# Kernel optimization log

Measured on AMD Instinct MI355X. Metric: run time of the kernel, lower is better.

Reference implementation:

```python
import jax, jax.numpy as jnp
import numpy as np

B, S, D, H, E = 8, 196, 768, 12, 8
HD = D // H  # 64
FF = 4 * D   # 3072
EPS = 1e-5


def setup_inputs() -> dict:
    key = jax.random.key(0)
    ks = jax.random.split(key, 12)
    s = 0.02
    inp = {
        'x': jax.random.normal(ks[0], (B, S, D), jnp.float32),
        'ln1_g': jnp.ones((D,), jnp.float32),
        'ln1_b': jnp.zeros((D,), jnp.float32),
        'Wq': jax.random.normal(ks[1], (D, D), jnp.float32) * s,
        'bq': jnp.zeros((D,), jnp.float32),
        'Wk': jax.random.normal(ks[2], (D, HD), jnp.float32) * s,
        'bk': jnp.zeros((HD,), jnp.float32),
        'Wv': jax.random.normal(ks[3], (D, HD), jnp.float32) * s,
        'bv': jnp.zeros((HD,), jnp.float32),
        'ln2_g': jnp.ones((D,), jnp.float32),
        'ln2_b': jnp.zeros((D,), jnp.float32),
        'Wg': jax.random.normal(ks[4], (D, E), jnp.float32) * s,
        'bg': jnp.zeros((E,), jnp.float32),
        'W1': jax.random.normal(ks[5], (E, D, FF), jnp.float32) * s,
        'b1': jnp.zeros((E, FF), jnp.float32),
        'W2': jax.random.normal(ks[6], (E, FF, D), jnp.float32) * s,
        'b2': jnp.zeros((E, D), jnp.float32),
    }
    return inp


def _layernorm(x, g, b):
    mu = jnp.mean(x, axis=-1, keepdims=True)
    var = jnp.var(x, axis=-1, keepdims=True)
    return (x - mu) * jax.lax.rsqrt(var + EPS) * g + b


def _rotate_half(x):
    x1, x2 = jnp.split(x, 2, axis=-1)
    return jnp.concatenate((-x2, x1), axis=-1)


def _rope(seq_len):
    inv_freq = 1.0 / (10000.0 ** (jnp.arange(0, HD, 2, dtype=jnp.float32) / HD))
    freqs = jnp.arange(seq_len, dtype=jnp.float32)[:, None] * inv_freq[None, :]
    emb = jnp.concatenate((freqs, freqs), axis=-1)  # [S, HD]
    return emb[None, :, None, :]  # [1, S, 1, HD]


def _attention(x, Wq, bq, Wk, bk, Wv, bv):
    b, s, _ = x.shape
    q = (x @ Wq + bq).reshape(b, s, H, HD)
    k = (x @ Wk + bk).reshape(b, s, 1, HD)
    v = (x @ Wv + bv).reshape(b, s, 1, HD)
    k = jnp.broadcast_to(k, (b, s, H, HD))
    v = jnp.broadcast_to(v, (b, s, H, HD))
    pe = _rope(s)
    cos, sin = jnp.cos(pe), jnp.sin(pe)
    q = q * cos + _rotate_half(q) * sin
    k = k * cos + _rotate_half(k) * sin
    scale = HD ** -0.5
    # NOTE: faithful to source -- matmul over the last two dims of [b,s,h,d],
    # i.e. attention across HEADS, not sequence positions.
    attn = jnp.einsum('bshd,bsgd->bshg', q, k) * scale
    attn = jax.nn.softmax(attn, axis=-1)
    out = jnp.einsum('bshg,bsgd->bshd', attn, v)
    return out.reshape(b, s, H * HD)


def _moe(x, Wg, bg, W1, b1, W2, b2):
    b, s, d = x.shape
    xt = x.reshape(-1, d)  # [T, D]
    gates = jax.nn.softmax(xt @ Wg + bg, axis=-1)
    top1 = jnp.argmax(gates, axis=-1)  # topk(k=2)[:,0] == argmax
    out = jnp.zeros_like(xt)
    for e in range(E):  # small fixed expert count
        h = jax.nn.gelu(xt @ W1[e] + b1[e], approximate=False)
        y = h @ W2[e] + b2[e]
        out = jnp.where((top1 == e)[:, None], y, out)
    return out.reshape(b, s, d)


def reference(x, ln1_g, ln1_b, Wq, bq, Wk, bk, Wv, bv, ln2_g, ln2_b, Wg, bg, W1, b1, W2, b2):
    res = x
    h = _layernorm(x, ln1_g, ln1_b)
    h = _attention(h, Wq, bq, Wk, bk, Wv, bv)
    x = res + h
    res = x
    h = _layernorm(x, ln2_g, ln2_b)
    h = _moe(h, Wg, bg, W1, b1, W2, b2)
    return res + h
```

## Files before the change

kernel.cpp:

```cpp
#include <hip/hip_runtime.h>
#include <hip/hip_bf16.h>


typedef unsigned short u16;
typedef short bf16x8_t __attribute__((ext_vector_type(8)));
typedef unsigned short u16x4_t __attribute__((ext_vector_type(4)));
typedef float f32x4_t  __attribute__((ext_vector_type(4)));

#define T_TOK 1568
#define DM 768
#define HD 64
#define FF 3072
#define NE 8

#define OFF_CNT   0
#define OFF_BUCK  256
#define OFF_V     (OFF_BUCK + NE*T_TOK*4)
#define OFF_H1    (OFF_V + T_TOK*HD*4)
#define OFF_H2    (OFF_H1 + T_TOK*DM*2)
#define OFF_HMID  (OFF_H2 + T_TOK*DM*2)

__device__ __forceinline__ u16 f2bf(float f) {
    return __builtin_bit_cast(u16, __float2bfloat16(f));
}
__device__ __forceinline__ float bf2f(u16 h) {
    unsigned u = ((unsigned)h) << 16;
    return __builtin_bit_cast(float, u);
}
__device__ __forceinline__ float gelu_f(float x) {
    return 0.5f * x * (1.0f + erff(x * 0.70710678118654752440f));
}

#define SFENCE() __builtin_amdgcn_sched_barrier(0)
#define RAW_BAR() __builtin_amdgcn_s_barrier()

__global__ __launch_bounds__(64) void k_ln1(const float* __restrict__ x,
                                            const float* __restrict__ g1,
                                            const float* __restrict__ b1,
                                            u16* __restrict__ h1) {
    int t = blockIdx.x, lane = threadIdx.x;
    const float* xp = x + (size_t)t * DM;
    f32x4_t xv[3];
    float s = 0.0f;
#pragma unroll
    for (int i = 0; i < 3; i++) {
        xv[i] = *(const f32x4_t*)&xp[4 * lane + 256 * i];
        s += xv[i][0] + xv[i][1] + xv[i][2] + xv[i][3];
    }
#pragma unroll
    for (int m = 1; m < 64; m <<= 1) s += __shfl_xor(s, m);
    float mu = s * (1.0f / DM);
    float vs = 0.0f;
#pragma unroll
    for (int i = 0; i < 3; i++)
#pragma unroll
        for (int m = 0; m < 4; m++) { float d = xv[i][m] - mu; vs += d * d; }
#pragma unroll
    for (int m = 1; m < 64; m <<= 1) vs += __shfl_xor(vs, m);
    float rs = rsqrtf(vs * (1.0f / DM) + 1e-5f);
    u16* hp = h1 + (size_t)t * DM;
#pragma unroll
    for (int i = 0; i < 3; i++) {
        int c = 4 * lane + 256 * i;
        f32x4_t gg = *(const f32x4_t*)&g1[c];
        f32x4_t bb = *(const f32x4_t*)&b1[c];
        u16x4_t hb;
#pragma unroll
        for (int m = 0; m < 4; m++) hb[m] = f2bf((xv[i][m] - mu) * rs * gg[m] + bb[m]);
        *(u16x4_t*)&hp[c] = hb;
    }
}

__global__ __launch_bounds__(256) void k_vproj(
        const u16* __restrict__ h1, const float* __restrict__ Wv,
        const float* __restrict__ bv, float* __restrict__ vws) {
    __shared__ __align__(16) u16 Bh[64 * 72];
    __shared__ __align__(16) u16 Bl[64 * 72];
    int m0 = blockIdx.x * 64;
    int tid = threadIdx.x, lane = tid & 63, wid = tid >> 6;
    int bn = tid & 63, bkg = tid >> 6;
    int lr = lane & 15, q = lane >> 4;
    int row = m0 + wid * 16 + lr;
    if (row >= T_TOK) row = T_TOK - 1;
    const u16* ap = h1 + (size_t)row * DM;

    f32x4_t acc[4];
#pragma unroll
    for (int ni = 0; ni < 4; ni++) acc[ni] = (f32x4_t){0.f, 0.f, 0.f, 0.f};

    bf16x8_t aP[2], aQ[2];
    float bP[16], bQ[16];

#define G_LOAD_A(SA, KT) { \
    int k0_ = (KT) * 64; \
    SA[0] = *(const bf16x8_t*)&ap[k0_ + q * 8]; \
    SA[1] = *(const bf16x8_t*)&ap[k0_ + 32 + q * 8]; \
}
#define G_LOAD_B(SB, KT) { \
    const float* bp_ = Wv + (size_t)((KT) * 64 + bkg * 16) * HD + bn; \
    _Pragma("unroll") \
    for (int kk = 0; kk < 16; kk++) SB[kk] = bp_[(size_t)kk * HD]; \
}
#define STORE_B(SB) { \
    bf16x8_t h0_, h1_, l0_, l1_; \
    _Pragma("unroll") \
    for (int kk = 0; kk < 8; kk++) { \
        float w0 = SB[kk], w1 = SB[kk + 8]; \
        u16 hh0 = f2bf(w0), hh1 = f2bf(w1); \
        h0_[kk] = (short)hh0; h1_[kk] = (short)hh1; \
        l0_[kk] = (short)f2bf(w0 - bf2f(hh0)); \
        l1_[kk] = (short)f2bf(w1 - bf2f(hh1)); \
    } \
    *(bf16x8_t*)&Bh[bn * 72 + bkg * 16] = h0_; \
    *(bf16x8_t*)&Bh[bn * 72 + bkg * 16 + 8] = h1_; \
    *(bf16x8_t*)&Bl[bn * 72 + bkg * 16] = l0_; \
    *(bf16x8_t*)&Bl[bn * 72 + bkg * 16 + 8] = l1_; \
}
#define MFMA_TILE(SA) { \
    _Pragma("unroll") \
    for (int s = 0; s < 2; s++) { \
        bf16x8_t bh_[4], bl_[4]; \
        _Pragma("unroll") \
        for (int ni = 0; ni < 4; ni++) { \
            bh_[ni] = *(const bf16x8_t*)&Bh[(ni * 16 + lr) * 72 + s * 32 + q * 8]; \
            bl_[ni] = *(const bf16x8_t*)&Bl[(ni * 16 + lr) * 72 + s * 32 + q * 8]; \
        } \
        _Pragma("unroll") \
        for (int ni = 0; ni < 4; ni++) { \
            acc[ni] = __builtin_amdgcn_mfma_f32_16x16x32_bf16( \
                SA[s], bh_[ni], acc[ni], 0, 0, 0); \
            acc[ni] = __builtin_amdgcn_mfma_f32_16x16x32_bf16( \
                SA[s], bl_[ni], acc[ni], 0, 0, 0); \
        } \
    } \
}
#define PHASE(SA, SB, PKT) { \
    SFENCE(); RAW_BAR(); SFENCE(); \
    STORE_B(SB) \
    asm volatile("s_waitcnt lgkmcnt(0)" ::: "memory"); \
    SFENCE(); RAW_BAR(); SFENCE(); \
    if ((PKT) < 12) G_LOAD_B(SB, PKT) \
    MFMA_TILE(SA) \
    if ((PKT) < 12) G_LOAD_A(SA, PKT) \
}

    G_LOAD_A(aP, 0) G_LOAD_B(bP, 0)
    G_LOAD_A(aQ, 1) G_LOAD_B(bQ, 1)
    for (int kt = 0; kt < 12; kt += 2) {
        PHASE(aP, bP, kt + 2)
        PHASE(aQ, bQ, kt + 3)
    }
#undef G_LOAD_A
#undef G_LOAD_B
#undef STORE_B
#undef MFMA_TILE
#undef PHASE

#pragma unroll
    for (int ni = 0; ni < 4; ni++) {
        float bb = bv[ni * 16 + lr];
#pragma unroll
        for (int r = 0; r < 4; r++) {
            int i = m0 + wid * 16 + q * 4 + r;
            if (i < T_TOK) vws[(size_t)i * HD + ni * 16 + lr] = acc[ni][r] + bb;
        }
    }
}

__global__ __launch_bounds__(64) void k_gate(
        const float* __restrict__ x, const float* __restrict__ vws,
        const float* __restrict__ g2, const float* __restrict__ b2g,
        const float* __restrict__ Wg, const float* __restrict__ bg,
        const float* __restrict__ b2moe,
        u16* __restrict__ h2, float* __restrict__ out,
        int* __restrict__ cnt, int* __restrict__ buck) {
    int t = blockIdx.x, lane = threadIdx.x;
    int sl = lane & 15;
    const float* xp = x + (size_t)t * DM;
    f32x4_t xv[3];
    f32x4_t vv = *(const f32x4_t*)&vws[(size_t)t * HD + 4 * sl];
    float s2 = 0.0f;
#pragma unroll
    for (int i = 0; i < 3; i++) {
        xv[i] = *(const f32x4_t*)&xp[4 * lane + 256 * i];
#pragma unroll
        for (int m = 0; m < 4; m++) { xv[i][m] += vv[m]; s2 += xv[i][m]; }
    }
#pragma unroll
    for (int m = 1; m < 64; m <<= 1) s2 += __shfl_xor(s2, m);
    float mu2 = s2 * (1.0f / DM);
    float vs2 = 0.0f;
#pragma unroll
    for (int i = 0; i < 3; i++)
#pragma unroll
        for (int m = 0; m < 4; m++) { float d = xv[i][m] - mu2; vs2 += d * d; }
#pragma unroll
    for (int m = 1; m < 64; m <<= 1) vs2 += __shfl_xor(vs2, m);
    float rs2 = rsqrtf(vs2 * (1.0f / DM) + 1e-5f);

    float le[NE];
#pragma unroll
    for (int e = 0; e < NE; e++) le[e] = 0.0f;
    u16* h2p = h2 + (size_t)t * DM;
#pragma unroll
    for (int i = 0; i < 3; i++) {
        int c = 4 * lane + 256 * i;
        f32x4_t gg = *(const f32x4_t*)&g2[c];
        f32x4_t bb = *(const f32x4_t*)&b2g[c];
        float h[4];
        u16x4_t hb;
#pragma unroll
        for (int m = 0; m < 4; m++) {
            h[m] = (xv[i][m] - mu2) * rs2 * gg[m] + bb[m];
            hb[m] = f2bf(h[m]);
        }
        *(u16x4_t*)&h2p[c] = hb;
#pragma unroll
        for (int m = 0; m < 4; m++) {
            f32x4_t w0 = *(const f32x4_t*)&Wg[(size_t)(c + m) * NE];
            f32x4_t w1 = *(const f32x4_t*)&Wg[(size_t)(c + m) * NE + 4];
            le[0] += h[m] * w0[0]; le[1] += h[m] * w0[1];
            le[2] += h[m] * w0[2]; le[3] += h[m] * w0[3];
            le[4] += h[m] * w1[0]; le[5] += h[m] * w1[1];
            le[6] += h[m] * w1[2]; le[7] += h[m] * w1[3];
        }
    }
#pragma unroll
    for (int e = 0; e < NE; e++) {
#pragma unroll
        for (int m = 1; m < 64; m <<= 1) le[e] += __shfl_xor(le[e], m);
    }
    float best = le[0] + bg[0]; int be = 0;
#pragma unroll
    for (int e = 1; e < NE; e++) {
        float qv = le[e] + bg[e];
        if (qv > best) { best = qv; be = e; }
    }
    if (lane == 0) {
        int pos = atomicAdd(&cnt[be], 1);
        buck[be * T_TOK + pos] = t;
    }
    float* op = out + (size_t)t * DM;
    const float* bp = b2moe + (size_t)be * DM;
#pragma unroll
    for (int i = 0; i < 3; i++) {
        int c = 4 * lane + 256 * i;
        f32x4_t bbv = *(const f32x4_t*)&bp[c];
        f32x4_t o;
#pragma unroll
        for (int m = 0; m < 4; m++) o[m] = xv[i][m] + bbv[m];
        *(f32x4_t*)&op[c] = o;
    }
}

__global__ __launch_bounds__(256, 4) void k_moe_gemm1(
        const u16* __restrict__ h2, const float* __restrict__ W1,
        const float* __restrict__ b1, const int* __restrict__ cnt,
        const int* __restrict__ buck, u16* __restrict__ hmid) {
    int nt = blockIdx.x, e = blockIdx.y, mt = blockIdx.z;
    int cnte = cnt[e];
    int m0 = mt * 64;
    if (m0 >= cnte) return;
    int n0 = nt * 64;
    const float* W1e = W1 + (size_t)e * DM * FF;
    __shared__ __align__(16) u16 Bs[64 * 72];
    int tid = threadIdx.x, lane = tid & 63, wid = tid >> 6;
    int bn = tid & 63, bkg = tid >> 6;
    int lr = lane & 15, q = lane >> 4;

    int arow = m0 + wid * 16 + lr;
    if (arow >= cnte) arow = cnte - 1;
    const u16* ap = h2 + (size_t)buck[e * T_TOK + arow] * DM;

    f32x4_t acc[4];
#pragma unroll
    for (int ni = 0; ni < 4; ni++) acc[ni] = (f32x4_t){0.f, 0.f, 0.f, 0.f};

    bf16x8_t aP[2], aQ[2];
    float bP[16], bQ[16];

#define G_LOAD_A(SA, KT) { \
    int k0_ = (KT) * 64; \
    SA[0] = *(const bf16x8_t*)&ap[k0_ + q * 8]; \
    SA[1] = *(const bf16x8_t*)&ap[k0_ + 32 + q * 8]; \
}
#define G_LOAD_B(SB, KT) { \
    const float* bp_ = W1e + (size_t)((KT) * 64 + bkg * 16) * FF + n0 + bn; \
    _Pragma("unroll") \
    for (int kk = 0; kk < 16; kk++) SB[kk] = bp_[(size_t)kk * FF]; \
}
#define STORE_B(SB) { \
    bf16x8_t p0_, p1_; \
    _Pragma("unroll") \
    for (int kk = 0; kk < 8; kk++) { \
        p0_[kk] = (short)f2bf(SB[kk]); \
        p1_[kk] = (short)f2bf(SB[kk + 8]); \
    } \
    *(bf16x8_t*)&Bs[bn * 72 + bkg * 16] = p0_; \
    *(bf16x8_t*)&Bs[bn * 72 + bkg * 16 + 8] = p1_; \
}
#define MFMA_TILE(SA) { \
    _Pragma("unroll") \
    for (int s = 0; s < 2; s++) { \
        bf16x8_t bfr[4]; \
        _Pragma("unroll") \
        for (int ni = 0; ni < 4; ni++) \
            bfr[ni] = *(const bf16x8_t*)&Bs[(ni * 16 + lr) * 72 + s * 32 + q * 8]; \
        _Pragma("unroll") \
        for (int ni = 0; ni < 4; ni++) \
            acc[ni] = __builtin_amdgcn_mfma_f32_16x16x32_bf16( \
                SA[s], bfr[ni], acc[ni], 0, 0, 0); \
    } \
}
#define PHASE(SA, SB, PKT) { \
    SFENCE(); RAW_BAR(); SFENCE(); \
    STORE_B(SB) \
    asm volatile("s_waitcnt lgkmcnt(0)" ::: "memory"); \
    SFENCE(); RAW_BAR(); SFENCE(); \
    if ((PKT) < 12) G_LOAD_B(SB, PKT) \
    MFMA_TILE(SA) \
    if ((PKT) < 12) G_LOAD_A(SA, PKT) \
}

    G_LOAD_A(aP, 0) G_LOAD_B(bP, 0)
    G_LOAD_A(aQ, 1) G_LOAD_B(bQ, 1)
    for (int kt = 0; kt < 12; kt += 2) {
        PHASE(aP, bP, kt + 2)
        PHASE(aQ, bQ, kt + 3)
    }
#undef G_LOAD_A
#undef G_LOAD_B
#undef STORE_B
#undef MFMA_TILE
#undef PHASE

    float bias[4];
#pragma unroll
    for (int ni = 0; ni < 4; ni++) bias[ni] = b1[(size_t)e * FF + n0 + ni * 16 + lr];
#pragma unroll
    for (int r = 0; r < 4; r++) {
        int i = m0 + wid * 16 + q * 4 + r;
        if (i < cnte) {
            int t = buck[e * T_TOK + i];
            size_t base = (size_t)t * FF + n0;
#pragma unroll
            for (int ni = 0; ni < 4; ni++)
                hmid[base + ni * 16 + lr] = f2bf(gelu_f(acc[ni][r] + bias[ni]));
        }
    }
}

__global__ __launch_bounds__(256, 4) void k_moe_gemm2(
        const u16* __restrict__ hmid, const float* __restrict__ W2,
        const int* __restrict__ cnt, const int* __restrict__ buck,
        float* __restrict__ out) {
    int nt = blockIdx.x, e = blockIdx.y, z = blockIdx.z;
    int kc = z & 3, mt = z >> 2;
    int cnte = cnt[e];
    int m0 = mt * 64;
    if (m0 >= cnte) return;
    int n0 = nt * 64;
    int kbase = kc * (FF / 4);
    const float* W2e = W2 + (size_t)e * FF * DM;
    __shared__ __align__(16) u16 Bs[64 * 72];
    int tid = threadIdx.x, lane = tid & 63, wid = tid >> 6;
    int bn = tid & 63, bkg = tid >> 6;
    int lr = lane & 15, q = lane >> 4;

    int arow = m0 + wid * 16 + lr;
    if (arow >= cnte) arow = cnte - 1;
    const u16* ap = hmid + (size_t)buck[e * T_TOK + arow] * FF + kbase;

    f32x4_t acc[4];
#pragma unroll
    for (int ni = 0; ni < 4; ni++) acc[ni] = (f32x4_t){0.f, 0.f, 0.f, 0.f};

    bf16x8_t aP[2], aQ[2];
    float bP[16], bQ[16];

#define G_LOAD_A(SA, KT) { \
    int k0_ = (KT) * 64; \
    SA[0] = *(const bf16x8_t*)&ap[k0_ + q * 8]; \
    SA[1] = *(const bf16x8_t*)&ap[k0_ + 32 + q * 8]; \
}
#define G_LOAD_B(SB, KT) { \
    const float* bp_ = W2e + (size_t)(kbase + (KT) * 64 + bkg * 16) * DM + n0 + bn; \
    _Pragma("unroll") \
    for (int kk = 0; kk < 16; kk++) SB[kk] = bp_[(size_t)kk * DM]; \
}
#define STORE_B(SB) { \
    bf16x8_t p0_, p1_; \
    _Pragma("unroll") \
    for (int kk = 0; kk < 8; kk++) { \
        p0_[kk] = (short)f2bf(SB[kk]); \
        p1_[kk] = (short)f2bf(SB[kk + 8]); \
    } \
    *(bf16x8_t*)&Bs[bn * 72 + bkg * 16] = p0_; \
    *(bf16x8_t*)&Bs[bn * 72 + bkg * 16 + 8] = p1_; \
}
#define MFMA_TILE(SA) { \
    _Pragma("unroll") \
    for (int s = 0; s < 2; s++) { \
        bf16x8_t bfr[4]; \
        _Pragma("unroll") \
        for (int ni = 0; ni < 4; ni++) \
            bfr[ni] = *(const bf16x8_t*)&Bs[(ni * 16 + lr) * 72 + s * 32 + q * 8]; \
        _Pragma("unroll") \
        for (int ni = 0; ni < 4; ni++) \
            acc[ni] = __builtin_amdgcn_mfma_f32_16x16x32_bf16( \
                SA[s], bfr[ni], acc[ni], 0, 0, 0); \
    } \
}
#define PHASE(SA, SB, PKT) { \
    SFENCE(); RAW_BAR(); SFENCE(); \
    STORE_B(SB) \
    asm volatile("s_waitcnt lgkmcnt(0)" ::: "memory"); \
    SFENCE(); RAW_BAR(); SFENCE(); \
    if ((PKT) < 12) G_LOAD_B(SB, PKT) \
    MFMA_TILE(SA) \
    if ((PKT) < 12) G_LOAD_A(SA, PKT) \
}

    G_LOAD_A(aP, 0) G_LOAD_B(bP, 0)
    G_LOAD_A(aQ, 1) G_LOAD_B(bQ, 1)
    for (int kt = 0; kt < 12; kt += 2) {
        PHASE(aP, bP, kt + 2)
        PHASE(aQ, bQ, kt + 3)
    }
#undef G_LOAD_A
#undef G_LOAD_B
#undef STORE_B
#undef MFMA_TILE
#undef PHASE

#pragma unroll
    for (int r = 0; r < 4; r++) {
        int i = m0 + wid * 16 + q * 4 + r;
        if (i < cnte) {
            int t = buck[e * T_TOK + i];
            size_t base = (size_t)t * DM + n0;
#pragma unroll
            for (int ni = 0; ni < 4; ni++)
                atomicAdd(&out[base + ni * 16 + lr], acc[ni][r]);
        }
    }
}

extern "C" void kernel_launch(void* const* d_in, const int* in_sizes, int n_in,
                              void* d_out, int out_size, void* d_ws, size_t ws_size,
                              hipStream_t stream) {
    const float* x    = (const float*)d_in[0];
    const float* ln1g = (const float*)d_in[1];
    const float* ln1b = (const float*)d_in[2];
    const float* Wv   = (const float*)d_in[7];
    const float* bv   = (const float*)d_in[8];
    const float* ln2g = (const float*)d_in[9];
    const float* ln2b = (const float*)d_in[10];
    const float* Wg   = (const float*)d_in[11];
    const float* bg   = (const float*)d_in[12];
    const float* W1   = (const float*)d_in[13];
    const float* b1   = (const float*)d_in[14];
    const float* W2   = (const float*)d_in[15];
    const float* b2   = (const float*)d_in[16];

    char* ws = (char*)d_ws;
    int*   cnt  = (int*)(ws + OFF_CNT);
    int*   buck = (int*)(ws + OFF_BUCK);
    float* vws  = (float*)(ws + OFF_V);
    u16*   h1   = (u16*)(ws + OFF_H1);
    u16*   h2   = (u16*)(ws + OFF_H2);
    u16*   hmid = (u16*)(ws + OFF_HMID);
    float* out  = (float*)d_out;

    hipMemsetAsync(cnt, 0, NE * sizeof(int), stream);
    k_ln1<<<T_TOK, 64, 0, stream>>>(x, ln1g, ln1b, h1);
    k_vproj<<<(T_TOK + 63) / 64, 256, 0, stream>>>(h1, Wv, bv, vws);
    k_gate<<<T_TOK, 64, 0, stream>>>(x, vws, ln2g, ln2b, Wg, bg, b2,
                                     h2, out, cnt, buck);
    k_moe_gemm1<<<dim3(FF / 64, NE, 25), 256, 0, stream>>>(h2, W1, b1, cnt, buck, hmid);
    k_moe_gemm2<<<dim3(DM / 64, NE, 100), 256, 0, stream>>>(hmid, W2, cnt, buck, out);
}
```

Measured before the change: 295.3 us.

## Double MoE GEMM M-tile to 128 rows and vectorize weight loads

Both MoE expert GEMMs now give each block 128 token rows instead of 64, with each wave computing two 16-row MFMA sub-tiles. Each fp32 weight tile converted to bf16 in LDS is therefore reused across twice as many rows, which halves the redundant global weight reads and conversion work. Weight loads also change from scalar strided loads to float2 loads covering two adjacent columns. The cost is more accumulator and A-fragment registers (launch bounds lowered from 4 to 3 waves) and fewer blocks, which can leave CUs underused when an expert has few tokens.

Measured after the change: 284.4 us. -3.7%, faster.

```diff
diff --git a/kernel.cpp b/kernel.cpp
--- a/kernel.cpp
+++ b/kernel.cpp
@@ -6,6 +6,7 @@
 typedef short bf16x8_t __attribute__((ext_vector_type(8)));
 typedef unsigned short u16x4_t __attribute__((ext_vector_type(4)));
 typedef float f32x4_t  __attribute__((ext_vector_type(4)));
+typedef float f32x2_t  __attribute__((ext_vector_type(2)));
 
 #define T_TOK 1568
 #define DM 768
@@ -253,51 +254,61 @@
     }
 }
 
-__global__ __launch_bounds__(256, 4) void k_moe_gemm1(
+__global__ __launch_bounds__(256, 3) void k_moe_gemm1(
         const u16* __restrict__ h2, const float* __restrict__ W1,
         const float* __restrict__ b1, const int* __restrict__ cnt,
         const int* __restrict__ buck, u16* __restrict__ hmid) {
     int nt = blockIdx.x, e = blockIdx.y, mt = blockIdx.z;
     int cnte = cnt[e];
-    int m0 = mt * 64;
+    int m0 = mt * 128;
     if (m0 >= cnte) return;
     int n0 = nt * 64;
     const float* W1e = W1 + (size_t)e * DM * FF;
     __shared__ __align__(16) u16 Bs[64 * 72];
     int tid = threadIdx.x, lane = tid & 63, wid = tid >> 6;
-    int bn = tid & 63, bkg = tid >> 6;
+    int n2 = (tid & 31) * 2, kg = tid >> 5;
     int lr = lane & 15, q = lane >> 4;
 
-    int arow = m0 + wid * 16 + lr;
-    if (arow >= cnte) arow = cnte - 1;
-    const u16* ap = h2 + (size_t)buck[e * T_TOK + arow] * DM;
-
-    f32x4_t acc[4];
-#pragma unroll
-    for (int ni = 0; ni < 4; ni++) acc[ni] = (f32x4_t){0.f, 0.f, 0.f, 0.f};
-
-    bf16x8_t aP[2], aQ[2];
+    int ar0 = m0 + wid * 32 + lr;
+    int ar1 = ar0 + 16;
+    if (ar0 >= cnte) ar0 = cnte - 1;
+    if (ar1 >= cnte) ar1 = cnte - 1;
+    const u16* ap0 = h2 + (size_t)buck[e * T_TOK + ar0] * DM;
+    const u16* ap1 = h2 + (size_t)buck[e * T_TOK + ar1] * DM;
+
+    f32x4_t acc[2][4];
+#pragma unroll
+    for (int mi = 0; mi < 2; mi++)
+#pragma unroll
+        for (int ni = 0; ni < 4; ni++) acc[mi][ni] = (f32x4_t){0.f, 0.f, 0.f, 0.f};
+
+    bf16x8_t aP[4], aQ[4];
     float bP[16], bQ[16];
 
 #define G_LOAD_A(SA, KT) { \
     int k0_ = (KT) * 64; \
-    SA[0] = *(const bf16x8_t*)&ap[k0_ + q * 8]; \
-    SA[1] = *(const bf16x8_t*)&ap[k0_ + 32 + q * 8]; \
+    SA[0] = *(const bf16x8_t*)&ap0[k0_ + q * 8]; \
+    SA[1] = *(const bf16x8_t*)&ap1[k0_ + q * 8]; \
+    SA[2] = *(const bf16x8_t*)&ap0[k0_ + 32 + q * 8]; \
+    SA[3] = *(const bf16x8_t*)&ap1[k0_ + 32 + q * 8]; \
 }
 #define G_LOAD_B(SB, KT) { \
-    const float* bp_ = W1e + (size_t)((KT) * 64 + bkg * 16) * FF + n0 + bn; \
-    _Pragma("unroll") \
-    for (int kk = 0; kk < 16; kk++) SB[kk] = bp_[(size_t)kk * FF]; \
+    const float* bp_ = W1e + (size_t)((KT) * 64 + kg * 8) * FF + n0 + n2; \
+    _Pragma("unroll") \
+    for (int r = 0; r < 8; r++) { \
+        f32x2_t t_ = *(const f32x2_t*)&bp_[(size_t)r * FF]; \
+        SB[r] = t_[0]; SB[8 + r] = t_[1]; \
+    } \
 }
 #define STORE_B(SB) { \
     bf16x8_t p0_, p1_; \
     _Pragma("unroll") \
-    for (int kk = 0; kk < 8; kk++) { \
-        p0_[kk] = (short)f2bf(SB[kk]); \
-        p1_[kk] = (short)f2bf(SB[kk + 8]); \
-    } \
-    *(bf16x8_t*)&Bs[bn * 72 + bkg * 16] = p0_; \
-    *(bf16x8_t*)&Bs[bn * 72 + bkg * 16 + 8] = p1_; \
+    for (int r = 0; r < 8; r++) { \
+        p0_[r] = (short)f2bf(SB[r]); \
+        p1_[r] = (short)f2bf(SB[8 + r]); \
+    } \
+    *(bf16x8_t*)&Bs[n2 * 72 + kg * 8] = p0_; \
+    *(bf16x8_t*)&Bs[(n2 + 1) * 72 + kg * 8] = p1_; \
 }
 #define MFMA_TILE(SA) { \
     _Pragma("unroll") \
@@ -307,9 +318,11 @@
         for (int ni = 0; ni < 4; ni++) \
             bfr[ni] = *(const bf16x8_t*)&Bs[(ni * 16 + lr) * 72 + s * 32 + q * 8]; \
         _Pragma("unroll") \
-        for (int ni = 0; ni < 4; ni++) \
-            acc[ni] = __builtin_amdgcn_mfma_f32_16x16x32_bf16( \
-                SA[s], bfr[ni], acc[ni], 0, 0, 0); \
+        for (int mi = 0; mi < 2; mi++) \
+            _Pragma("unroll") \
+            for (int ni = 0; ni < 4; ni++) \
+                acc[mi][ni] = __builtin_amdgcn_mfma_f32_16x16x32_bf16( \
+                    SA[s * 2 + mi], bfr[ni], acc[mi][ni], 0, 0, 0); \
     } \
 }
 #define PHASE(SA, SB, PKT) { \
@@ -338,65 +351,78 @@
 #pragma unroll
     for (int ni = 0; ni < 4; ni++) bias[ni] = b1[(size_t)e * FF + n0 + ni * 16 + lr];
 #pragma unroll
-    for (int r = 0; r < 4; r++) {
-        int i = m0 + wid * 16 + q * 4 + r;
-        if (i < cnte) {
-            int t = buck[e * T_TOK + i];
-            size_t base = (size_t)t * FF + n0;
-#pragma unroll
-            for (int ni = 0; ni < 4; ni++)
-                hmid[base + ni * 16 + lr] = f2bf(gelu_f(acc[ni][r] + bias[ni]));
+    for (int mi = 0; mi < 2; mi++) {
+#pragma unroll
+        for (int r = 0; r < 4; r++) {
+            int i = m0 + wid * 32 + mi * 16 + q * 4 + r;
+            if (i < cnte) {
+                int t = buck[e * T_TOK + i];
+                size_t base = (size_t)t * FF + n0;
+#pragma unroll
+                for (int ni = 0; ni < 4; ni++)
+                    hmid[base + ni * 16 + lr] = f2bf(gelu_f(acc[mi][ni][r] + bias[ni]));
+            }
         }
     }
 }
 
-__global__ __launch_bounds__(256, 4) void k_moe_gemm2(
+__global__ __launch_bounds__(256, 3) void k_moe_gemm2(
         const u16* __restrict__ hmid, const float* __restrict__ W2,
         const int* __restrict__ cnt, const int* __restrict__ buck,
         float* __restrict__ out) {
     int nt = blockIdx.x, e = blockIdx.y, z = blockIdx.z;
     int kc = z & 3, mt = z >> 2;
     int cnte = cnt[e];
-    int m0 = mt * 64;
+    int m0 = mt * 128;
     if (m0 >= cnte) return;
     int n0 = nt * 64;
     int kbase = kc * (FF / 4);
     const float* W2e = W2 + (size_t)e * FF * DM;
     __shared__ __align__(16) u16 Bs[64 * 72];
     int tid = threadIdx.x, lane = tid & 63, wid = tid >> 6;
-    int bn = tid & 63, bkg = tid >> 6;
+    int n2 = (tid & 31) * 2, kg = tid >> 5;
     int lr = lane & 15, q = lane >> 4;
 
-    int arow = m0 + wid * 16 + lr;
-    if (arow >= cnte) arow = cnte - 1;
-    const u16* ap = hmid + (size_t)buck[e * T_TOK + arow] * FF + kbase;
-
-    f32x4_t acc[4];
-#pragma unroll
-    for (int ni = 0; ni < 4; ni++) acc[ni] = (f32x4_t){0.f, 0.f, 0.f, 0.f};
-
-    bf16x8_t aP[2], aQ[2];
+    int ar0 = m0 + wid * 32 + lr;
+    int ar1 = ar0 + 16;
+    if (ar0 >= cnte) ar0 = cnte - 1;
+    if (ar1 >= cnte) ar1 = cnte - 1;
+    const u16* ap0 = hmid + (size_t)buck[e * T_TOK + ar0] * FF + kbase;
+    const u16* ap1 = hmid + (size_t)buck[e * T_TOK + ar1] * FF + kbase;
+
+    f32x4_t acc[2][4];
+#pragma unroll
+    for (int mi = 0; mi < 2; mi++)
+#pragma unroll
+        for (int ni = 0; ni < 4; ni++) acc[mi][ni] = (f32x4_t){0.f, 0.f, 0.f, 0.f};
+
+    bf16x8_t aP[4], aQ[4];
     float bP[16], bQ[16];
 
 #define G_LOAD_A(SA, KT) { \
     int k0_ = (KT) * 64; \
-    SA[0] = *(const bf16x8_t*)&ap[k0_ + q * 8]; \
-    SA[1] = *(const bf16x8_t*)&ap[k0_ + 32 + q * 8]; \
+    SA[0] = *(const bf16x8_t*)&ap0[k0_ + q * 8]; \
+    SA[1] = *(const bf16x8_t*)&ap1[k0_ + q * 8]; \
+    SA[2] = *(const bf16x8_t*)&ap0[k0_ + 32 + q * 8]; \
+    SA[3] = *(const bf16x8_t*)&ap1[k0_ + 32 + q * 8]; \
 }
 #define G_LOAD_B(SB, KT) { \
-    const float* bp_ = W2e + (size_t)(kbase + (KT) * 64 + bkg * 16) * DM + n0 + bn; \
-    _Pragma("unroll") \
-    for (int kk = 0; kk < 16; kk++) SB[kk] = bp_[(size_t)kk * DM]; \
+    const float* bp_ = W2e + (size_t)(kbase + (KT) * 64 + kg * 8) * DM + n0 + n2; \
+    _Pragma("unroll") \
+    for (int r = 0; r < 8; r++) { \
+        f32x2_t t_ = *(const f32x2_t*)&bp_[(size_t)r * DM]; \
+        SB[r] = t_[0]; SB[8 + r] = t_[1]; \
+    } \
 }
 #define STORE_B(SB) { \
     bf16x8_t p0_, p1_; \
     _Pragma("unroll") \
-    for (int kk = 0; kk < 8; kk++) { \
-        p0_[kk] = (short)f2bf(SB[kk]); \
-        p1_[kk] = (short)f2bf(SB[kk + 8]); \
-    } \
-    *(bf16x8_t*)&Bs[bn * 72 + bkg * 16] = p0_; \
-    *(bf16x8_t*)&Bs[bn * 72 + bkg * 16 + 8] = p1_; \
+    for (int r = 0; r < 8; r++) { \
+        p0_[r] = (short)f2bf(SB[r]); \
+        p1_[r] = (short)f2bf(SB[8 + r]); \
+    } \
+    *(bf16x8_t*)&Bs[n2 * 72 + kg * 8] = p0_; \
+    *(bf16x8_t*)&Bs[(n2 + 1) * 72 + kg * 8] = p1_; \
 }
 #define MFMA_TILE(SA) { \
     _Pragma("unroll") \
@@ -406,9 +432,11 @@
         for (int ni = 0; ni < 4; ni++) \
             bfr[ni] = *(const bf16x8_t*)&Bs[(ni * 16 + lr) * 72 + s * 32 + q * 8]; \
         _Pragma("unroll") \
-        for (int ni = 0; ni < 4; ni++) \
-            acc[ni] = __builtin_amdgcn_mfma_f32_16x16x32_bf16( \
-                SA[s], bfr[ni], acc[ni], 0, 0, 0); \
+        for (int mi = 0; mi < 2; mi++) \
+            _Pragma("unroll") \
+            for (int ni = 0; ni < 4; ni++) \
+                acc[mi][ni] = __builtin_amdgcn_mfma_f32_16x16x32_bf16( \
+                    SA[s * 2 + mi], bfr[ni], acc[mi][ni], 0, 0, 0); \
     } \
 }
 #define PHASE(SA, SB, PKT) { \
@@ -434,14 +462,17 @@
 #undef PHASE
 
 #pragma unroll
-    for (int r = 0; r < 4; r++) {
-        int i = m0 + wid * 16 + q * 4 + r;
-        if (i < cnte) {
-            int t = buck[e * T_TOK + i];
-            size_t base = (size_t)t * DM + n0;
-#pragma unroll
-            for (int ni = 0; ni < 4; ni++)
-                atomicAdd(&out[base + ni * 16 + lr], acc[ni][r]);
+    for (int mi = 0; mi < 2; mi++) {
+#pragma unroll
+        for (int r = 0; r < 4; r++) {
+            int i = m0 + wid * 32 + mi * 16 + q * 4 + r;
+            if (i < cnte) {
+                int t = buck[e * T_TOK + i];
+                size_t base = (size_t)t * DM + n0;
+#pragma unroll
+                for (int ni = 0; ni < 4; ni++)
+                    atomicAdd(&out[base + ni * 16 + lr], acc[mi][ni][r]);
+            }
         }
     }
 }
@@ -477,6 +508,6 @@
     k_vproj<<<(T_TOK + 63) / 64, 256, 0, stream>>>(h1, Wv, bv, vws);
     k_gate<<<T_TOK, 64, 0, stream>>>(x, vws, ln2g, ln2b, Wg, bg, b2,
                                      h2, out, cnt, buck);
-    k_moe_gemm1<<<dim3(FF / 64, NE, 25), 256, 0, stream>>>(h2, W1, b1, cnt, buck, hmid);
-    k_moe_gemm2<<<dim3(DM / 64, NE, 100), 256, 0, stream>>>(hmid, W2, cnt, buck, out);
-}
+    k_moe_gemm1<<<dim3(FF / 64, NE, 13), 256, 0, stream>>>(h2, W1, b1, cnt, buck, hmid);
+    k_moe_gemm2<<<dim3(DM / 64, NE, 52), 256, 0, stream>>>(hmid, W2, cnt, buck, out);
+}
```
